# Kernel tuning notes

Hardware: AMD Instinct MI355X
Metric: run time of the kernel (lower is better)

The kernel has to match this reference:

```python
import jax, jax.numpy as jnp
import numpy as np

N, E = 50000, 800000
IN_DIM, HID, H1, H2, NCLS = 512, 64, 4, 1, 40
NEG_SLOPE = 0.2


def gat_conv(x, src, dst, W, att_src, att_dst, b, heads, ch):
    # x: [N, F_in]; W: [F_in, heads*ch]; att_*: [heads, ch]; b: [heads*ch]
    n = x.shape[0]
    h = (x @ W).reshape(n, heads, ch)                      # [N,H,C]
    a_s = jnp.einsum('nhc,hc->nh', h, att_src)             # [N,H]
    a_d = jnp.einsum('nhc,hc->nh', h, att_dst)             # [N,H]
    e = jax.nn.leaky_relu(a_s[src] + a_d[dst], NEG_SLOPE)  # [E,H]
    # segment softmax over incoming edges of each destination node
    m = jax.ops.segment_max(e, dst, num_segments=n)        # [N,H]
    ex = jnp.exp(e - m[dst])
    s = jax.ops.segment_sum(ex, dst, num_segments=n)       # [N,H]
    alpha = ex / (s[dst] + 1e-16)                          # [E,H]
    out = jax.ops.segment_sum(alpha[:, :, None] * h[src], dst, num_segments=n)
    return out.reshape(n, heads * ch) + b


def setup_inputs() -> dict:
    key = jax.random.key(0)
    ks = jax.random.split(key, 10)
    glorot = lambda k, shp: jax.random.normal(k, shp, jnp.float32) * jnp.sqrt(2.0 / (shp[0] + shp[-1]))
    return {
        'x': jax.random.normal(ks[0], (N, IN_DIM), jnp.float32),
        'edge_index': jax.random.randint(ks[1], (2, E), 0, N, jnp.int64),
        'W1': glorot(ks[2], (IN_DIM, H1 * HID)),
        'att_src1': glorot(ks[3], (H1, HID)),
        'att_dst1': glorot(ks[4], (H1, HID)),
        'b1': jnp.zeros((H1 * HID,), jnp.float32),
        'W2': glorot(ks[5], (H1 * HID, H2 * NCLS)),
        'att_src2': glorot(ks[6], (H2, NCLS)),
        'att_dst2': glorot(ks[7], (H2, NCLS)),
        'b2': jnp.zeros((H2 * NCLS,), jnp.float32),
    }


def reference(x, edge_index, W1, att_src1, att_dst1, b1, W2, att_src2, att_dst2, b2):
    n = x.shape[0]
    loops = jnp.arange(n, dtype=edge_index.dtype)
    src = jnp.concatenate([edge_index[0], loops])  # add self loops (PyG default)
    dst = jnp.concatenate([edge_index[1], loops])
    # dropout layers are identity in eval mode
    h = gat_conv(x, src, dst, W1, att_src1, att_dst1, b1, H1, HID)
    h = jax.nn.elu(h)
    out = gat_conv(h, src, dst, W2, att_src2, att_dst2, b2, H2, NCLS)
    return jax.nn.log_softmax(out, axis=1)
```

## Files before the change

### kernel.cpp

```cpp
#include <hip/hip_runtime.h>
#include <math.h>
#include <stdint.h>


typedef short bf16x8 __attribute__((ext_vector_type(8)));
typedef float f32x4  __attribute__((ext_vector_type(4)));

static __device__ __forceinline__ float leaky(float x){ return x > 0.f ? x : 0.2f*x; }
static __device__ __forceinline__ unsigned short f2bf(float f){
  uint32_t u = __float_as_uint(f);
  uint32_t r = u + 0x7fffu + ((u >> 16) & 1u);
  return (unsigned short)(r >> 16);
}
static __device__ __forceinline__ float bf2f(unsigned short u){
  return __uint_as_float(((uint32_t)u) << 16);
}

__global__ void k_cvt_w(const float* __restrict__ W, unsigned short* __restrict__ wt,
                        const float* __restrict__ W2, unsigned short* __restrict__ wt2,
                        int* __restrict__ deg, int n){
  int i = blockIdx.x*blockDim.x + threadIdx.x;
  if (i < n) deg[i] = 0;
  if (i < 256*64){
    int col = i & 255, kg = i >> 8;
    int kt = kg >> 2, kq = kg & 3;
    unsigned short* dst = wt + ((size_t)kt*1024 + kq*256 + col)*8;
    bf16x8 p;
    #pragma unroll
    for (int j=0;j<8;j++) p[j] = (short)f2bf(W[(size_t)(kg*8+j)*256 + col]);
    *(bf16x8*)dst = p;
  } else if (i < 256*64 + 2048) {
    int i2 = i - 256*64;
    int col = i2 & 63, kg = i2 >> 6;
    bf16x8 p;
    #pragma unroll
    for (int j=0;j<8;j++)
      p[j] = (col < 40) ? (short)f2bf(W2[(size_t)(kg*8+j)*40 + col]) : (short)0;
    *(bf16x8*)(wt2 + (size_t)i2*8) = p;
  }
}

__global__ void k_count(const int* __restrict__ ei, int E, int n, int* __restrict__ deg){
  int i = blockIdx.x*blockDim.x + threadIdx.x;
  int tot = E + n;
  if (i >= tot) return;
  int dst = (i < E) ? ei[E + i] : (i - E);
  atomicAdd(&deg[dst], 1);
}

__global__ __launch_bounds__(256) void k_scan_a(const int* __restrict__ deg,
    int* __restrict__ rowstart, int* __restrict__ bsum, int n){
  __shared__ int sm[256];
  int b = blockIdx.x, t = threadIdx.x;
  int i = b*256 + t;
  int v = (i < n) ? deg[i] : 0;
  sm[t] = v;
  __syncthreads();
  for (int off=1; off<256; off<<=1){
    int u = (t >= off) ? sm[t-off] : 0;
    __syncthreads();
    sm[t] += u;
    __syncthreads();
  }
  if (i < n) rowstart[i+1] = sm[t];
  if (t == 255) bsum[b] = sm[255];
}
__global__ __launch_bounds__(256) void k_scan_b(int* __restrict__ bsum, int nb){
  __shared__ int sm[256];
  int t = threadIdx.x;
  int v = (t < nb) ? bsum[t] : 0;
  sm[t] = v;
  __syncthreads();
  for (int off=1; off<256; off<<=1){
    int u = (t >= off) ? sm[t-off] : 0;
    __syncthreads();
    sm[t] += u;
    __syncthreads();
  }
  if (t < nb) bsum[t] = sm[t] - v;
}
__global__ __launch_bounds__(256) void k_scan_c(int* __restrict__ rowstart,
    const int* __restrict__ bsum, int* __restrict__ cur, int n){
  int b = blockIdx.x, t = threadIdx.x;
  int i = b*256 + t;
  if (i < n){ rowstart[i+1] += bsum[b]; cur[i] = 0; }
  if (i == 0) rowstart[0] = 0;
}

__global__ __launch_bounds__(256, 4) void k_gemm1_mfma(const float* __restrict__ X,
                                                    const unsigned short* __restrict__ WT,
                                                    const float* __restrict__ SW,
                                                    const float* __restrict__ DW,
                                                    unsigned short* __restrict__ Cb,
                                                    float* __restrict__ as1,
                                                    float* __restrict__ ad1, int M){
  __shared__ __align__(16) unsigned short lA[2][2048];
  __shared__ __align__(16) unsigned short lB[2][4096];
  const int t = threadIdx.x;
  const int lane = t & 63, w = t >> 6;
  const int wx = w & 1, wy = w >> 1;
  const int row0 = blockIdx.x * 64, col0 = blockIdx.y * 128;

  f32x4 acc[2][4];
  #pragma unroll
  for (int i=0;i<2;i++)
    #pragma unroll
    for (int j=0;j<4;j++)
      #pragma unroll
      for (int r=0;r<4;r++) acc[i][j][r] = 0.f;

  const int rA = w*16 + (lane & 15);
  const int kA = lane >> 4;
  const float* xA = X + (size_t)min(row0 + rA, M-1)*512 + kA*8;
  const int aChunk = kA*64 + rA;

  const int c0 = t, c1 = t + 256;
  const unsigned short* bB0 = WT + ((size_t)(c0>>7)*256 + col0 + (c0&127))*8;
  const unsigned short* bB1 = WT + ((size_t)(c1>>7)*256 + col0 + (c1&127))*8;

  const int fkq = lane >> 4, li = lane & 15;

  float4 pA0, pA1, qA0, qA1;
  uint4  pB0, pB1, qB0, qB1;

#define LOAD_T(A0,A1,B0,B1, T) do{ \
  A0 = *(const float4*)(xA + (T)*32); \
  A1 = *(const float4*)(xA + (T)*32 + 4); \
  B0 = *(const uint4*)(bB0 + (size_t)(T)*8192); \
  B1 = *(const uint4*)(bB1 + (size_t)(T)*8192); }while(0)

#define WRITE_T(NXT, A0,A1,B0,B1) do{ \
  bf16x8 p0; \
  p0[0]=(short)f2bf(A0.x); p0[1]=(short)f2bf(A0.y); p0[2]=(short)f2bf(A0.z); p0[3]=(short)f2bf(A0.w); \
  p0[4]=(short)f2bf(A1.x); p0[5]=(short)f2bf(A1.y); p0[6]=(short)f2bf(A1.z); p0[7]=(short)f2bf(A1.w); \
  *(bf16x8*)&lA[NXT][aChunk*8] = p0; \
  *(uint4*)&lB[NXT][c0*8] = B0; \
  *(uint4*)&lB[NXT][c1*8] = B1; }while(0)

#define BARRIER() do{ \
  asm volatile("s_waitcnt lgkmcnt(0)" ::: "memory"); \
  __builtin_amdgcn_s_barrier(); \
  asm volatile("" ::: "memory"); }while(0)

#define STEP(T, CUR, A0,A1,B0,B1) do{ \
  bf16x8 af[2], bfr[4]; \
  _Pragma("unroll") \
  for (int i=0;i<2;i++) \
    af[i]  = *(const bf16x8*)&lA[CUR][(fkq*64 + wx*32 + i*16 + li)*8]; \
  _Pragma("unroll") \
  for (int j=0;j<4;j++) \
    bfr[j] = *(const bf16x8*)&lB[CUR][(fkq*128 + wy*64 + j*16 + li)*8]; \
  _Pragma("unroll") \
  for (int i=0;i<2;i++) \
    _Pragma("unroll") \
    for (int j=0;j<4;j++) \
      acc[i][j] = __builtin_amdgcn_mfma_f32_16x16x32_bf16(af[i], bfr[j], acc[i][j], 0, 0, 0); \
  if ((T) < 15){ \
    WRITE_T((CUR)^1, A0,A1,B0,B1); \
    if ((T) <= 12) LOAD_T(A0,A1,B0,B1, (T)+3); \
    BARRIER(); \
  } \
}while(0)

  {
    LOAD_T(pA0,pA1,pB0,pB1, 0);
    WRITE_T(0, pA0,pA1,pB0,pB1);
    LOAD_T(pA0,pA1,pB0,pB1, 1);
    LOAD_T(qA0,qA1,qB0,qB1, 2);
    BARRIER();
  }

  #pragma unroll
  for (int tt = 0; tt < 8; ++tt){
    STEP(2*tt,   (0), pA0,pA1,pB0,pB1);
    STEP(2*tt+1, (1), qA0,qA1,qB0,qB1);
  }

#undef STEP
#undef BARRIER
#undef WRITE_T
#undef LOAD_T

  #pragma unroll
  for (int i=0;i<2;i++){
    #pragma unroll
    for (int r=0;r<4;r++){
      int row = row0 + wx*32 + i*16 + fkq*4 + r;
      if (row < M){
        #pragma unroll
        for (int j=0;j<4;j++)
          Cb[(size_t)row*256 + col0 + wy*64 + j*16 + li] = f2bf(acc[i][j][r]);
      }
    }
  }

  const int hw = (int)blockIdx.y*2 + wy;
  float sv[4], dv[4];
  #pragma unroll
  for (int j=0;j<4;j++){
    sv[j] = SW[hw*64 + j*16 + li];
    dv[j] = DW[hw*64 + j*16 + li];
  }
  #pragma unroll
  for (int i=0;i<2;i++){
    #pragma unroll
    for (int r=0;r<4;r++){
      float ps = acc[i][0][r]*sv[0] + acc[i][1][r]*sv[1] + acc[i][2][r]*sv[2] + acc[i][3][r]*sv[3];
      float pd = acc[i][0][r]*dv[0] + acc[i][1][r]*dv[1] + acc[i][2][r]*dv[2] + acc[i][3][r]*dv[3];
      #pragma unroll
      for (int o=1;o<16;o<<=1){ ps += __shfl_xor(ps,o); pd += __shfl_xor(pd,o); }
      int row = row0 + wx*32 + i*16 + fkq*4 + r;
      if (li == 0 && row < M){
        as1[row*4 + hw] = ps;
        ad1[row*4 + hw] = pd;
      }
    }
  }
}

__global__ void k_fill(const int* __restrict__ ei, int E, int n,
                       const int* __restrict__ rowstart, int* __restrict__ cur,
                       int* __restrict__ csr,
                       const float* __restrict__ as1, const float* __restrict__ ad1,
                       float* __restrict__ exbuf){
  int i = blockIdx.x*blockDim.x + threadIdx.x;
  int tot = E + n;
  if (i >= tot) return;
  int src, dst;
  if (i < E){ src = ei[i]; dst = ei[E+i]; } else { src = i - E; dst = src; }
  int pos = atomicAdd(&cur[dst], 1);
  int slot = rowstart[dst] + pos;
  csr[slot] = src;
  float4 a = *(const float4*)(as1 + (size_t)src*4);
  float4 d = *(const float4*)(ad1 + (size_t)dst*4);
  float4 ex;
  ex.x = __expf(fminf(leaky(a.x + d.x), 80.f));
  ex.y = __expf(fminf(leaky(a.y + d.y), 80.f));
  ex.z = __expf(fminf(leaky(a.z + d.z), 80.f));
  ex.w = __expf(fminf(leaky(a.w + d.w), 80.f));
  *(float4*)(exbuf + (size_t)slot*4) = ex;
}

__global__ __launch_bounds__(256) void k_agg1(const unsigned short* __restrict__ h1b,
    const float* __restrict__ exbuf,
    const int* __restrict__ rowstart, const int* __restrict__ csr,
    const float* __restrict__ b1, unsigned short* __restrict__ hactb, int n){
  int lane = threadIdx.x & 63;
  int node = blockIdx.x*4 + (threadIdx.x >> 6);
  if (node >= n) return;
  int lo = __builtin_amdgcn_readfirstlane(rowstart[node]);
  int hi = __builtin_amdgcn_readfirstlane(rowstart[node+1]);
  int h = lane >> 4;
  const float* exb = exbuf + h;
  float ax=0.f, ay=0.f, az=0.f, aw=0.f, psum=0.f;
  int e = lo;
  for (; e + 7 < hi; e += 8){
    int s0 = csr[e],   s1 = csr[e+1], s2 = csr[e+2], s3 = csr[e+3];
    int s4 = csr[e+4], s5 = csr[e+5], s6 = csr[e+6], s7 = csr[e+7];
    float e0 = exb[(size_t)e*4],     e1 = exb[(size_t)(e+1)*4],
          e2 = exb[(size_t)(e+2)*4], e3 = exb[(size_t)(e+3)*4],
          e4 = exb[(size_t)(e+4)*4], e5 = exb[(size_t)(e+5)*4],
          e6 = exb[(size_t)(e+6)*4], e7 = exb[(size_t)(e+7)*4];
    ushort4 u0 = *(const ushort4*)(h1b + (size_t)s0*256 + lane*4);
    ushort4 u1 = *(const ushort4*)(h1b + (size_t)s1*256 + lane*4);
    ushort4 u2 = *(const ushort4*)(h1b + (size_t)s2*256 + lane*4);
    ushort4 u3 = *(const ushort4*)(h1b + (size_t)s3*256 + lane*4);
    ushort4 u4 = *(const ushort4*)(h1b + (size_t)s4*256 + lane*4);
    ushort4 u5 = *(const ushort4*)(h1b + (size_t)s5*256 + lane*4);
    ushort4 u6 = *(const ushort4*)(h1b + (size_t)s6*256 + lane*4);
    ushort4 u7 = *(const ushort4*)(h1b + (size_t)s7*256 + lane*4);
    ax += e0*bf2f(u0.x) + e1*bf2f(u1.x) + e2*bf2f(u2.x) + e3*bf2f(u3.x)
        + e4*bf2f(u4.x) + e5*bf2f(u5.x) + e6*bf2f(u6.x) + e7*bf2f(u7.x);
    ay += e0*bf2f(u0.y) + e1*bf2f(u1.y) + e2*bf2f(u2.y) + e3*bf2f(u3.y)
        + e4*bf2f(u4.y) + e5*bf2f(u5.y) + e6*bf2f(u6.y) + e7*bf2f(u7.y);
    az += e0*bf2f(u0.z) + e1*bf2f(u1.z) + e2*bf2f(u2.z) + e3*bf2f(u3.z)
        + e4*bf2f(u4.z) + e5*bf2f(u5.z) + e6*bf2f(u6.z) + e7*bf2f(u7.z);
    aw += e0*bf2f(u0.w) + e1*bf2f(u1.w) + e2*bf2f(u2.w) + e3*bf2f(u3.w)
        + e4*bf2f(u4.w) + e5*bf2f(u5.w) + e6*bf2f(u6.w) + e7*bf2f(u7.w);
    psum += (e0+e1+e2+e3) + (e4+e5+e6+e7);
  }
  for (; e < hi; ++e){
    int s0 = csr[e];
    float e0 = exb[(size_t)e*4];
    ushort4 u0 = *(const ushort4*)(h1b + (size_t)s0*256 + lane*4);
    ax += e0*bf2f(u0.x); ay += e0*bf2f(u0.y); az += e0*bf2f(u0.z); aw += e0*bf2f(u0.w);
    psum += e0;
  }
  float inv = 1.f/(psum + 1e-16f);
  float4 bv = *(const float4*)(b1 + lane*4);
  float o0 = ax*inv + bv.x, o1 = ay*inv + bv.y, o2 = az*inv + bv.z, o3 = aw*inv + bv.w;
  ushort4 r;
  r.x = f2bf(o0 > 0.f ? o0 : expm1f(o0));
  r.y = f2bf(o1 > 0.f ? o1 : expm1f(o1));
  r.z = f2bf(o2 > 0.f ? o2 : expm1f(o2));
  r.w = f2bf(o3 > 0.f ? o3 : expm1f(o3));
  *(ushort4*)(hactb + (size_t)node*256 + lane*4) = r;
}

__global__ __launch_bounds__(256, 4) void k_gemm2_mfma(const unsigned short* __restrict__ A,
    const unsigned short* __restrict__ WT2, const float* __restrict__ sw,
    const float* __restrict__ dw, unsigned short* __restrict__ Cb,
    float* __restrict__ as2, float* __restrict__ ad2, int M){
  __shared__ __align__(16) unsigned short lA[2][2048];
  __shared__ __align__(16) unsigned short lB[2][2048];
  const int t = threadIdx.x;
  const int lane = t & 63, w = t >> 6;
  const int row0 = blockIdx.x * 64;

  f32x4 acc[4];
  #pragma unroll
  for (int j=0;j<4;j++)
    #pragma unroll
    for (int r=0;r<4;r++) acc[j][r] = 0.f;

  const int rA = w*16 + (lane & 15);
  const int kA = lane >> 4;
  const unsigned short* pA = A + (size_t)min(row0 + rA, M-1)*256 + kA*8;
  const int aChunk = kA*64 + rA;
  const unsigned short* pB = WT2 + (size_t)t*8;

  const int fkq = lane >> 4, li = lane & 15;

  uint4 pAv, pBv, qAv, qBv;

#define LOAD_T(AV,BV, T) do{ \
  AV = *(const uint4*)(pA + (T)*32); \
  BV = *(const uint4*)(pB + (size_t)(T)*2048); }while(0)

#define WRITE_T(NXT, AV,BV) do{ \
  *(uint4*)&lA[NXT][aChunk*8] = AV; \
  *(uint4*)&lB[NXT][t*8] = BV; }while(0)

#define BARRIER() do{ \
  asm volatile("s_waitcnt lgkmcnt(0)" ::: "memory"); \
  __builtin_amdgcn_s_barrier(); \
  asm volatile("" ::: "memory"); }while(0)

#define STEP(T, CUR, AV,BV) do{ \
  bf16x8 af = *(const bf16x8*)&lA[CUR][(fkq*64 + w*16 + li)*8]; \
  bf16x8 bfr[4]; \
  _Pragma("unroll") \
  for (int j=0;j<4;j++) \
    bfr[j] = *(const bf16x8*)&lB[CUR][(fkq*64 + j*16 + li)*8]; \
  _Pragma("unroll") \
  for (int j=0;j<4;j++) \
    acc[j] = __builtin_amdgcn_mfma_f32_16x16x32_bf16(af, bfr[j], acc[j], 0, 0, 0); \
  if ((T) < 7){ \
    WRITE_T((CUR)^1, AV,BV); \
    if ((T) <= 4) LOAD_T(AV,BV, (T)+3); \
    BARRIER(); \
  } \
}while(0)

  {
    LOAD_T(pAv,pBv, 0);
    WRITE_T(0, pAv,pBv);
    LOAD_T(pAv,pBv, 1);
    LOAD_T(qAv,qBv, 2);
    BARRIER();
  }
  STEP(0, 0, pAv,pBv);
  STEP(1, 1, qAv,qBv);
  STEP(2, 0, pAv,pBv);
  STEP(3, 1, qAv,qBv);
  STEP(4, 0, pAv,pBv);
  STEP(5, 1, qAv,qBv);
  STEP(6, 0, pAv,pBv);
  STEP(7, 1, qAv,qBv);

#undef STEP
#undef BARRIER
#undef WRITE_T
#undef LOAD_T

  float swv[4], dwv[4];
  #pragma unroll
  for (int j=0;j<4;j++){
    int col = j*16 + li;
    swv[j] = (col < 40) ? sw[col] : 0.f;
    dwv[j] = (col < 40) ? dw[col] : 0.f;
  }
  #pragma unroll
  for (int r=0;r<4;r++){
    int grow = row0 + w*16 + fkq*4 + r;
    if (grow < M){
      Cb[(size_t)grow*40 + li]      = f2bf(acc[0][r]);
      Cb[(size_t)grow*40 + 16 + li] = f2bf(acc[1][r]);
      if (li < 8) Cb[(size_t)grow*40 + 32 + li] = f2bf(acc[2][r]);
    }
    float ps = acc[0][r]*swv[0] + acc[1][r]*swv[1] + acc[2][r]*swv[2] + acc[3][r]*swv[3];
    float pd = acc[0][r]*dwv[0] + acc[1][r]*dwv[1] + acc[2][r]*dwv[2] + acc[3][r]*dwv[3];
    #pragma unroll
    for (int o=1;o<16;o<<=1){ ps += __shfl_xor(ps,o); pd += __shfl_xor(pd,o); }
    if (li == 0 && grow < M){ as2[grow] = ps; ad2[grow] = pd; }
  }
}

__global__ __launch_bounds__(256) void k_agg2(const unsigned short* __restrict__ h2b,
    const float* __restrict__ as2, const float* __restrict__ ad2,
    const int* __restrict__ rowstart, const int* __restrict__ csr,
    const float* __restrict__ b2, float* __restrict__ out, int n){
  int lane = threadIdx.x & 63;
  int node = blockIdx.x*4 + (threadIdx.x >> 6);
  if (node >= n) return;
  int lo = __builtin_amdgcn_readfirstlane(rowstart[node]);
  int hi = __builtin_amdgcn_readfirstlane(rowstart[node+1]);
  float adn = ad2[node];
  bool act = lane < 40;
  float acc = 0.f, psum = 0.f;
  int e = lo;
  for (; e + 7 < hi; e += 8){
    int s0 = csr[e],   s1 = csr[e+1], s2 = csr[e+2], s3 = csr[e+3];
    int s4 = csr[e+4], s5 = csr[e+5], s6 = csr[e+6], s7 = csr[e+7];
    float e0 = __expf(fminf(leaky(as2[s0] + adn), 80.f));
    float e1 = __expf(fminf(leaky(as2[s1] + adn), 80.f));
    float e2 = __expf(fminf(leaky(as2[s2] + adn), 80.f));
    float e3 = __expf(fminf(leaky(as2[s3] + adn), 80.f));
    float e4 = __expf(fminf(leaky(as2[s4] + adn), 80.f));
    float e5 = __expf(fminf(leaky(as2[s5] + adn), 80.f));
    float e6 = __expf(fminf(leaky(as2[s6] + adn), 80.f));
    float e7 = __expf(fminf(leaky(as2[s7] + adn), 80.f));
    float h0 = act ? bf2f(h2b[(size_t)s0*40 + lane]) : 0.f;
    float h1 = act ? bf2f(h2b[(size_t)s1*40 + lane]) : 0.f;
    float h2 = act ? bf2f(h2b[(size_t)s2*40 + lane]) : 0.f;
    float h3 = act ? bf2f(h2b[(size_t)s3*40 + lane]) : 0.f;
    float h4 = act ? bf2f(h2b[(size_t)s4*40 + lane]) : 0.f;
    float h5 = act ? bf2f(h2b[(size_t)s5*40 + lane]) : 0.f;
    float h6 = act ? bf2f(h2b[(size_t)s6*40 + lane]) : 0.f;
    float h7 = act ? bf2f(h2b[(size_t)s7*40 + lane]) : 0.f;
    acc += e0*h0 + e1*h1 + e2*h2 + e3*h3 + e4*h4 + e5*h5 + e6*h6 + e7*h7;
    psum += (e0+e1+e2+e3) + (e4+e5+e6+e7);
  }
  for (; e < hi; ++e){
    int s0 = csr[e];
    float e0 = __expf(fminf(leaky(as2[s0] + adn), 80.f));
    acc += e0 * (act ? bf2f(h2b[(size_t)s0*40 + lane]) : 0.f);
    psum += e0;
  }
  float ov = acc/(psum + 1e-16f) + (act ? b2[lane] : 0.f);
  float v = act ? ov : -INFINITY;
  float mx = v;
  #pragma unroll
  for (int o=1;o<64;o<<=1) mx = fmaxf(mx, __shfl_xor(mx,o));
  float ev = act ? __expf(ov - mx) : 0.f;
  float se = ev;
  #pragma unroll
  for (int o=1;o<64;o<<=1) se += __shfl_xor(se,o);
  if (act) out[(size_t)node*40 + lane] = (ov - mx) - __logf(se);
}

extern "C" void kernel_launch(void* const* d_in, const int* in_sizes, int n_in,
                              void* d_out, int out_size, void* d_ws, size_t ws_size,
                              hipStream_t stream){
  const float* x   = (const float*)d_in[0];
  const int*   ei  = (const int*)d_in[1];
  const float* W1  = (const float*)d_in[2];
  const float* s1w = (const float*)d_in[3];
  const float* d1w = (const float*)d_in[4];
  const float* b1  = (const float*)d_in[5];
  const float* W2  = (const float*)d_in[6];
  const float* s2w = (const float*)d_in[7];
  const float* d2w = (const float*)d_in[8];
  const float* b2  = (const float*)d_in[9];
  float* out = (float*)d_out;

  const int N  = in_sizes[0] / 512;
  const int E  = in_sizes[1] / 2;
  const int Et = E + N;

  float* f = (float*)d_ws;
  unsigned short* h1b   = (unsigned short*)f;  f += (size_t)N*128;
  unsigned short* hactb = (unsigned short*)f;  f += (size_t)N*128;
  float* as1  = f;  f += (size_t)N*4;
  float* ad1  = f;  f += (size_t)N*4;
  float* as2  = f;  f += N;
  float* ad2  = f;  f += N;
  unsigned short* w1t = (unsigned short*)f;  f += 256*512/2;
  unsigned short* w2t = (unsigned short*)f;  f += 2048*8/2;
  unsigned short* h2b = (unsigned short*)f;  f += (size_t)N*40/2 + 64;
  float* exbuf = f;  f += (size_t)Et*4;
  int* ip = (int*)f;
  int* rowstart = ip;  ip += (N + 4) & ~3;
  int* deg      = ip;  ip += N;
  int* cur      = ip;  ip += N;
  int* csr      = ip;  ip += Et;
  int* bsum     = ip;  ip += 256;

  int nb4 = (N + 3) / 4;
  int nbs = (N + 255) / 256;
  k_cvt_w<<<nbs, 256, 0, stream>>>(W1, w1t, W2, w2t, deg, N);
  k_count<<<(Et+255)/256, 256, 0, stream>>>(ei, E, N, deg);
  k_scan_a<<<nbs, 256, 0, stream>>>(deg, rowstart, bsum, N);
  k_scan_b<<<1, 256, 0, stream>>>(bsum, nbs);
  k_scan_c<<<nbs, 256, 0, stream>>>(rowstart, bsum, cur, N);
  k_gemm1_mfma<<<dim3((N+63)/64, 2), 256, 0, stream>>>(x, w1t, s1w, d1w, h1b, as1, ad1, N);
  k_fill <<<(Et+255)/256, 256, 0, stream>>>(ei, E, N, rowstart, cur, csr, as1, ad1, exbuf);
  k_agg1 <<<nb4, 256, 0, stream>>>(h1b, exbuf, rowstart, csr, b1, hactb, N);
  k_gemm2_mfma<<<(N+63)/64, 256, 0, stream>>>(hactb, w2t, s2w, d2w, h2b, as2, ad2, N);
  k_agg2 <<<nb4, 256, 0, stream>>>(h2b, as2, ad2, rowstart, csr, b2, out, N);
}
```

Baseline: 413.9 us.

## Restage GEMM1 with full-K A tile and recompute edge exps in aggregation

GEMM1 now loads a 32-row x 512-K slab of X into LDS once, with a single barrier. Each wave reads its W1 fragments straight from global memory instead of double-buffering them through LDS, and one block covers all 256 output columns, so X is read only once. The per-edge exp buffer is removed: k_fill only builds the CSR, and k_agg1 recomputes the attention exponentials from as1/ad1 gathered by source. This trades writing and re-reading an E*4 float buffer for extra gathers and exp work in the aggregation. It also risks more global-memory pressure in the GEMM from B reads that are no longer shared through LDS.

```diff
diff --git a/kernel.cpp b/kernel.cpp
--- a/kernel.cpp
+++ b/kernel.cpp
@@ -94,12 +94,28 @@
                                                     unsigned short* __restrict__ Cb,
                                                     float* __restrict__ as1,
                                                     float* __restrict__ ad1, int M){
-  __shared__ __align__(16) unsigned short lA[2][2048];
-  __shared__ __align__(16) unsigned short lB[2][4096];
+  __shared__ __align__(16) unsigned short lA[16384];
   const int t = threadIdx.x;
   const int lane = t & 63, w = t >> 6;
-  const int wx = w & 1, wy = w >> 1;
-  const int row0 = blockIdx.x * 64, col0 = blockIdx.y * 128;
+  const int row0 = blockIdx.x * 32;
+
+  {
+    const int rs = t >> 3, g = t & 7;
+    const float* xrow = X + (size_t)min(row0 + rs, M-1)*512 + g*64;
+    #pragma unroll
+    for (int j=0;j<8;j++){
+      float4 a0 = *(const float4*)(xrow + j*8);
+      float4 a1 = *(const float4*)(xrow + j*8 + 4);
+      bf16x8 p;
+      p[0]=(short)f2bf(a0.x); p[1]=(short)f2bf(a0.y); p[2]=(short)f2bf(a0.z); p[3]=(short)f2bf(a0.w);
+      p[4]=(short)f2bf(a1.x); p[5]=(short)f2bf(a1.y); p[6]=(short)f2bf(a1.z); p[7]=(short)f2bf(a1.w);
+      *(bf16x8*)&lA[((g*8 + j)*32 + rs)*8] = p;
+    }
+  }
+  __syncthreads();
+
+  const int fkq = lane >> 4, li = lane & 15;
+  const unsigned short* pB = WT + ((size_t)fkq*256 + w*64 + li)*8;
 
   f32x4 acc[2][4];
   #pragma unroll
@@ -109,110 +125,48 @@
       #pragma unroll
       for (int r=0;r<4;r++) acc[i][j][r] = 0.f;
 
-  const int rA = w*16 + (lane & 15);
-  const int kA = lane >> 4;
-  const float* xA = X + (size_t)min(row0 + rA, M-1)*512 + kA*8;
-  const int aChunk = kA*64 + rA;
-
-  const int c0 = t, c1 = t + 256;
-  const unsigned short* bB0 = WT + ((size_t)(c0>>7)*256 + col0 + (c0&127))*8;
-  const unsigned short* bB1 = WT + ((size_t)(c1>>7)*256 + col0 + (c1&127))*8;
-
-  const int fkq = lane >> 4, li = lane & 15;
-
-  float4 pA0, pA1, qA0, qA1;
-  uint4  pB0, pB1, qB0, qB1;
-
-#define LOAD_T(A0,A1,B0,B1, T) do{ \
-  A0 = *(const float4*)(xA + (T)*32); \
-  A1 = *(const float4*)(xA + (T)*32 + 4); \
-  B0 = *(const uint4*)(bB0 + (size_t)(T)*8192); \
-  B1 = *(const uint4*)(bB1 + (size_t)(T)*8192); }while(0)
-
-#define WRITE_T(NXT, A0,A1,B0,B1) do{ \
-  bf16x8 p0; \
-  p0[0]=(short)f2bf(A0.x); p0[1]=(short)f2bf(A0.y); p0[2]=(short)f2bf(A0.z); p0[3]=(short)f2bf(A0.w); \
-  p0[4]=(short)f2bf(A1.x); p0[5]=(short)f2bf(A1.y); p0[6]=(short)f2bf(A1.z); p0[7]=(short)f2bf(A1.w); \
-  *(bf16x8*)&lA[NXT][aChunk*8] = p0; \
-  *(uint4*)&lB[NXT][c0*8] = B0; \
-  *(uint4*)&lB[NXT][c1*8] = B1; }while(0)
-
-#define BARRIER() do{ \
-  asm volatile("s_waitcnt lgkmcnt(0)" ::: "memory"); \
-  __builtin_amdgcn_s_barrier(); \
-  asm volatile("" ::: "memory"); }while(0)
-
-#define STEP(T, CUR, A0,A1,B0,B1) do{ \
-  bf16x8 af[2], bfr[4]; \
-  _Pragma("unroll") \
-  for (int i=0;i<2;i++) \
-    af[i]  = *(const bf16x8*)&lA[CUR][(fkq*64 + wx*32 + i*16 + li)*8]; \
-  _Pragma("unroll") \
-  for (int j=0;j<4;j++) \
-    bfr[j] = *(const bf16x8*)&lB[CUR][(fkq*128 + wy*64 + j*16 + li)*8]; \
-  _Pragma("unroll") \
-  for (int i=0;i<2;i++) \
-    _Pragma("unroll") \
-    for (int j=0;j<4;j++) \
-      acc[i][j] = __builtin_amdgcn_mfma_f32_16x16x32_bf16(af[i], bfr[j], acc[i][j], 0, 0, 0); \
-  if ((T) < 15){ \
-    WRITE_T((CUR)^1, A0,A1,B0,B1); \
-    if ((T) <= 12) LOAD_T(A0,A1,B0,B1, (T)+3); \
-    BARRIER(); \
-  } \
-}while(0)
-
-  {
-    LOAD_T(pA0,pA1,pB0,pB1, 0);
-    WRITE_T(0, pA0,pA1,pB0,pB1);
-    LOAD_T(pA0,pA1,pB0,pB1, 1);
-    LOAD_T(qA0,qA1,qB0,qB1, 2);
-    BARRIER();
-  }
-
-  #pragma unroll
-  for (int tt = 0; tt < 8; ++tt){
-    STEP(2*tt,   (0), pA0,pA1,pB0,pB1);
-    STEP(2*tt+1, (1), qA0,qA1,qB0,qB1);
-  }
-
-#undef STEP
-#undef BARRIER
-#undef WRITE_T
-#undef LOAD_T
-
+  #pragma unroll
+  for (int kt=0; kt<16; ++kt){
+    bf16x8 af0 = *(const bf16x8*)&lA[((kt*4 + fkq)*32 +      li)*8];
+    bf16x8 af1 = *(const bf16x8*)&lA[((kt*4 + fkq)*32 + 16 + li)*8];
+    const unsigned short* pbk = pB + (size_t)kt*8192;
+    bf16x8 b0 = *(const bf16x8*)(pbk);
+    bf16x8 b1 = *(const bf16x8*)(pbk + 128);
+    bf16x8 b2 = *(const bf16x8*)(pbk + 256);
+    bf16x8 b3 = *(const bf16x8*)(pbk + 384);
+    acc[0][0] = __builtin_amdgcn_mfma_f32_16x16x32_bf16(af0, b0, acc[0][0], 0,0,0);
+    acc[0][1] = __builtin_amdgcn_mfma_f32_16x16x32_bf16(af0, b1, acc[0][1], 0,0,0);
+    acc[0][2] = __builtin_amdgcn_mfma_f32_16x16x32_bf16(af0, b2, acc[0][2], 0,0,0);
+    acc[0][3] = __builtin_amdgcn_mfma_f32_16x16x32_bf16(af0, b3, acc[0][3], 0,0,0);
+    acc[1][0] = __builtin_amdgcn_mfma_f32_16x16x32_bf16(af1, b0, acc[1][0], 0,0,0);
+    acc[1][1] = __builtin_amdgcn_mfma_f32_16x16x32_bf16(af1, b1, acc[1][1], 0,0,0);
+    acc[1][2] = __builtin_amdgcn_mfma_f32_16x16x32_bf16(af1, b2, acc[1][2], 0,0,0);
+    acc[1][3] = __builtin_amdgcn_mfma_f32_16x16x32_bf16(af1, b3, acc[1][3], 0,0,0);
+  }
+
+  float sv[4], dv[4];
+  #pragma unroll
+  for (int j=0;j<4;j++){
+    sv[j] = SW[w*64 + j*16 + li];
+    dv[j] = DW[w*64 + j*16 + li];
+  }
   #pragma unroll
   for (int i=0;i<2;i++){
     #pragma unroll
     for (int r=0;r<4;r++){
-      int row = row0 + wx*32 + i*16 + fkq*4 + r;
+      int row = row0 + i*16 + fkq*4 + r;
       if (row < M){
         #pragma unroll
         for (int j=0;j<4;j++)
-          Cb[(size_t)row*256 + col0 + wy*64 + j*16 + li] = f2bf(acc[i][j][r]);
+          Cb[(size_t)row*256 + w*64 + j*16 + li] = f2bf(acc[i][j][r]);
       }
-    }
-  }
-
-  const int hw = (int)blockIdx.y*2 + wy;
-  float sv[4], dv[4];
-  #pragma unroll
-  for (int j=0;j<4;j++){
-    sv[j] = SW[hw*64 + j*16 + li];
-    dv[j] = DW[hw*64 + j*16 + li];
-  }
-  #pragma unroll
-  for (int i=0;i<2;i++){
-    #pragma unroll
-    for (int r=0;r<4;r++){
       float ps = acc[i][0][r]*sv[0] + acc[i][1][r]*sv[1] + acc[i][2][r]*sv[2] + acc[i][3][r]*sv[3];
       float pd = acc[i][0][r]*dv[0] + acc[i][1][r]*dv[1] + acc[i][2][r]*dv[2] + acc[i][3][r]*dv[3];
       #pragma unroll
       for (int o=1;o<16;o<<=1){ ps += __shfl_xor(ps,o); pd += __shfl_xor(pd,o); }
-      int row = row0 + wx*32 + i*16 + fkq*4 + r;
       if (li == 0 && row < M){
-        as1[row*4 + hw] = ps;
-        ad1[row*4 + hw] = pd;
+        as1[row*4 + w] = ps;
+        ad1[row*4 + w] = pd;
       }
     }
   }
@@ -220,29 +174,18 @@
 
 __global__ void k_fill(const int* __restrict__ ei, int E, int n,
                        const int* __restrict__ rowstart, int* __restrict__ cur,
-                       int* __restrict__ csr,
-                       const float* __restrict__ as1, const float* __restrict__ ad1,
-                       float* __restrict__ exbuf){
+                       int* __restrict__ csr){
   int i = blockIdx.x*blockDim.x + threadIdx.x;
   int tot = E + n;
   if (i >= tot) return;
   int src, dst;
   if (i < E){ src = ei[i]; dst = ei[E+i]; } else { src = i - E; dst = src; }
   int pos = atomicAdd(&cur[dst], 1);
-  int slot = rowstart[dst] + pos;
-  csr[slot] = src;
-  float4 a = *(const float4*)(as1 + (size_t)src*4);
-  float4 d = *(const float4*)(ad1 + (size_t)dst*4);
-  float4 ex;
-  ex.x = __expf(fminf(leaky(a.x + d.x), 80.f));
-  ex.y = __expf(fminf(leaky(a.y + d.y), 80.f));
-  ex.z = __expf(fminf(leaky(a.z + d.z), 80.f));
-  ex.w = __expf(fminf(leaky(a.w + d.w), 80.f));
-  *(float4*)(exbuf + (size_t)slot*4) = ex;
+  csr[rowstart[dst] + pos] = src;
 }
 
 __global__ __launch_bounds__(256) void k_agg1(const unsigned short* __restrict__ h1b,
-    const float* __restrict__ exbuf,
+    const float* __restrict__ as1, const float* __restrict__ ad1,
     const int* __restrict__ rowstart, const int* __restrict__ csr,
     const float* __restrict__ b1, unsigned short* __restrict__ hactb, int n){
   int lane = threadIdx.x & 63;
@@ -251,16 +194,20 @@
   int lo = __builtin_amdgcn_readfirstlane(rowstart[node]);
   int hi = __builtin_amdgcn_readfirstlane(rowstart[node+1]);
   int h = lane >> 4;
-  const float* exb = exbuf + h;
+  float adh = ad1[(size_t)node*4 + h];
   float ax=0.f, ay=0.f, az=0.f, aw=0.f, psum=0.f;
   int e = lo;
   for (; e + 7 < hi; e += 8){
     int s0 = csr[e],   s1 = csr[e+1], s2 = csr[e+2], s3 = csr[e+3];
     int s4 = csr[e+4], s5 = csr[e+5], s6 = csr[e+6], s7 = csr[e+7];
-    float e0 = exb[(size_t)e*4],     e1 = exb[(size_t)(e+1)*4],
-          e2 = exb[(size_t)(e+2)*4], e3 = exb[(size_t)(e+3)*4],
-          e4 = exb[(size_t)(e+4)*4], e5 = exb[(size_t)(e+5)*4],
-          e6 = exb[(size_t)(e+6)*4], e7 = exb[(size_t)(e+7)*4];
+    float e0 = __expf(fminf(leaky(as1[(size_t)s0*4 + h] + adh), 80.f));
+    float e1 = __expf(fminf(leaky(as1[(size_t)s1*4 + h] + adh), 80.f));
+    float e2 = __expf(fminf(leaky(as1[(size_t)s2*4 + h] + adh), 80.f));
+    float e3 = __expf(fminf(leaky(as1[(size_t)s3*4 + h] + adh), 80.f));
+    float e4 = __expf(fminf(leaky(as1[(size_t)s4*4 + h] + adh), 80.f));
+    float e5 = __expf(fminf(leaky(as1[(size_t)s5*4 + h] + adh), 80.f));
+    float e6 = __expf(fminf(leaky(as1[(size_t)s6*4 + h] + adh), 80.f));
+    float e7 = __expf(fminf(leaky(as1[(size_t)s7*4 + h] + adh), 80.f));
     ushort4 u0 = *(const ushort4*)(h1b + (size_t)s0*256 + lane*4);
     ushort4 u1 = *(const ushort4*)(h1b + (size_t)s1*256 + lane*4);
     ushort4 u2 = *(const ushort4*)(h1b + (size_t)s2*256 + lane*4);
@@ -281,7 +228,7 @@
   }
   for (; e < hi; ++e){
     int s0 = csr[e];
-    float e0 = exb[(size_t)e*4];
+    float e0 = __expf(fminf(leaky(as1[(size_t)s0*4 + h] + adh), 80.f));
     ushort4 u0 = *(const ushort4*)(h1b + (size_t)s0*256 + lane*4);
     ax += e0*bf2f(u0.x); ay += e0*bf2f(u0.y); az += e0*bf2f(u0.z); aw += e0*bf2f(u0.w);
     psum += e0;
@@ -478,7 +425,6 @@
   unsigned short* w1t = (unsigned short*)f;  f += 256*512/2;
   unsigned short* w2t = (unsigned short*)f;  f += 2048*8/2;
   unsigned short* h2b = (unsigned short*)f;  f += (size_t)N*40/2 + 64;
-  float* exbuf = f;  f += (size_t)Et*4;
   int* ip = (int*)f;
   int* rowstart = ip;  ip += (N + 4) & ~3;
   int* deg      = ip;  ip += N;
@@ -493,9 +439,9 @@
   k_scan_a<<<nbs, 256, 0, stream>>>(deg, rowstart, bsum, N);
   k_scan_b<<<1, 256, 0, stream>>>(bsum, nbs);
   k_scan_c<<<nbs, 256, 0, stream>>>(rowstart, bsum, cur, N);
-  k_gemm1_mfma<<<dim3((N+63)/64, 2), 256, 0, stream>>>(x, w1t, s1w, d1w, h1b, as1, ad1, N);
-  k_fill <<<(Et+255)/256, 256, 0, stream>>>(ei, E, N, rowstart, cur, csr, as1, ad1, exbuf);
-  k_agg1 <<<nb4, 256, 0, stream>>>(h1b, exbuf, rowstart, csr, b1, hactb, N);
+  k_gemm1_mfma<<<(N+31)/32, 256, 0, stream>>>(x, w1t, s1w, d1w, h1b, as1, ad1, N);
+  k_fill <<<(Et+255)/256, 256, 0, stream>>>(ei, E, N, rowstart, cur, csr);
+  k_agg1 <<<nb4, 256, 0, stream>>>(h1b, as1, ad1, rowstart, csr, b1, hactb, N);
   k_gemm2_mfma<<<(N+63)/64, 256, 0, stream>>>(hactb, w2t, s2w, d2w, h2b, as2, ad2, N);
   k_agg2 <<<nb4, 256, 0, stream>>>(h2b, as2, ad2, rowstart, csr, b2, out, N);
 }
```

Measured after the change: 410.9 us. No clear change (-0.7%).
